# Performance work log

Hardware: AMD Instinct MI355X
Metric: run time of the kernel (lower is better)

## Reference

```python
import jax, jax.numpy as jnp
import numpy as np

ALPHA = 0.2        # LeakyReLU negative slope
MASK_VAL = -9e15   # matches torch zero_vec constant
B, N, F, H, D = 32, 1024, 64, 3, 16  # batch, nodes, in_features, heads, head_dim


def setup_inputs() -> dict:
    key = jax.random.key(0)
    k1, k2, k3 = jax.random.split(key, 3)
    h = jax.random.normal(k1, (B, N, F), dtype=jnp.float32)
    adj = jnp.ones((N, N), dtype=jnp.float32)  # fully-connected graph ('full')
    W = jax.random.normal(k2, (H, F, D), dtype=jnp.float32) * 0.15  # ~xavier gain 1.414
    a = jax.random.normal(k3, (H, 2 * D, 1), dtype=jnp.float32) * 0.25
    return {"h": h, "adj": adj, "W": W, "a": a}


def reference(h, adj, W, a):
    # Multi-head GAT, vectorized over heads (original loops over heads).
    d = W.shape[-1]
    Wh = jnp.einsum('bnf,hfd->bhnd', h, W)              # (B,H,N,D)
    a1 = a[:, :d, 0]                                    # (H,D) -> applies to source node i
    a2 = a[:, d:, 0]                                    # (H,D) -> applies to target node j
    s1 = jnp.einsum('bhnd,hd->bhn', Wh, a1)             # (B,H,N)
    s2 = jnp.einsum('bhnd,hd->bhn', Wh, a2)             # (B,H,N)
    # e[b,h,i,j] = LeakyReLU(a1.Wh_i + a2.Wh_j) -- equivalent to the repeat/concat trick
    e = jax.nn.leaky_relu(s1[..., :, None] + s2[..., None, :], ALPHA)  # (B,H,N,N)
    e = jnp.where(adj > 0, e, MASK_VAL)
    attn = jax.nn.softmax(e, axis=-1)                   # softmax over neighbors j
    out = jnp.einsum('bhij,bhjd->bhid', attn, Wh)       # (B,H,N,D)
    # concat heads along feature dim: (B,N,H*D)
    Bn, Nn = h.shape[0], h.shape[1]
    return out.transpose(0, 2, 1, 3).reshape(Bn, Nn, -1)
```

## Files before the change

kernel.cpp:

```cpp
#include <hip/hip_runtime.h>
#include <math.h>

constexpr int Bc = 32, Nn = 1024, Fc = 64, Hc = 3, Dc = 16;
constexpr float ALPHAc = 0.2f;
constexpr float L2E    = 1.44269504088896340736f;

__device__ __forceinline__ unsigned enc_f32(float x) {
    unsigned b = __builtin_bit_cast(unsigned, x);
    return (b & 0x80000000u) ? ~b : (b | 0x80000000u);
}
__device__ __forceinline__ float dec_f32(unsigned e) {
    unsigned b = (e & 0x80000000u) ? (e ^ 0x80000000u) : ~e;
    return __builtin_bit_cast(float, b);
}

template <int CTRL, int RMASK, bool BC>
__device__ __forceinline__ float dpp_acc(float x) {
    int s = __builtin_amdgcn_update_dpp(0, __builtin_bit_cast(int, x),
                                        CTRL, RMASK, 0xF, BC);
    return x + __builtin_bit_cast(float, s);
}
__device__ __forceinline__ float wave_incl_scan(float x) {
    x = dpp_acc<0x111, 0xF, true >(x);
    x = dpp_acc<0x112, 0xF, true >(x);
    x = dpp_acc<0x114, 0xF, true >(x);
    x = dpp_acc<0x118, 0xF, true >(x);
    x = dpp_acc<0x142, 0xa, false>(x);
    x = dpp_acc<0x143, 0xc, false>(x);
    return x;
}

__global__ __launch_bounds__(1024, 1) void gat_one(
    const float* __restrict__ hbuf, const float* __restrict__ W,
    const float* __restrict__ a, const float* __restrict__ adj,
    unsigned* __restrict__ rowful, float* Whf, float* __restrict__ out)
{
    __shared__ __align__(16) float    PS[1025 * 35];
    __shared__ __align__(16) unsigned skA[Nn], skB[Nn];
    __shared__ __align__(16) float    s2o[Nn];
    __shared__ float    wtot[16][34];
    __shared__ unsigned wmiss[16];

    int bh = blockIdx.x;
    int hh = bh % Hc, b = bh / Hc;
    int t  = threadIdx.x;
    int wv = t >> 6, lane = t & 63;

    int row0 = bh * 11;
    unsigned miss = 0;
#pragma unroll
    for (int rr = 0; rr < 11; ++rr) {
        int row = row0 + rr;
        if (row < Nn) {
            float av = adj[(size_t)row * Nn + t];
            miss |= (av > 0.f) ? 0u : (1u << rr);
        }
    }
#pragma unroll
    for (int off = 1; off < 64; off <<= 1)
        miss |= (unsigned)__shfl_xor((int)miss, off, 64);
    if (lane == 0) wmiss[wv] = miss;
    __syncthreads();
    if (t < 11) {
        int row = row0 + t;
        if (row < Nn) {
            unsigned m = 0;
#pragma unroll
            for (int w2 = 0; w2 < 16; ++w2) m |= wmiss[w2];
            unsigned full = ((m >> t) & 1u) ^ 1u;
            unsigned val  = 0x5AFE0000u | ((unsigned)row << 1) | full;
            __hip_atomic_store(&rowful[row], val, __ATOMIC_RELAXED,
                               __HIP_MEMORY_SCOPE_AGENT);
        }
    }

    const float4* h4 = (const float4*)(hbuf + ((size_t)b * Nn + t) * Fc);
    const float*  Wp = W + (size_t)hh * Fc * Dc;

    float acc[Dc];
#pragma unroll
    for (int d = 0; d < Dc; ++d) acc[d] = 0.f;

#pragma unroll
    for (int q = 0; q < Fc / 4; ++q) {
        float4 hv = h4[q];
#pragma unroll
        for (int c = 0; c < 4; ++c) {
            float hv1 = (c == 0) ? hv.x : (c == 1) ? hv.y : (c == 2) ? hv.z : hv.w;
            const float4* wrp = (const float4*)(Wp + (4 * q + c) * Dc);
#pragma unroll
            for (int u = 0; u < 4; ++u) {
                float4 wq = wrp[u];
                acc[4*u+0] = fmaf(hv1, wq.x, acc[4*u+0]);
                acc[4*u+1] = fmaf(hv1, wq.y, acc[4*u+1]);
                acc[4*u+2] = fmaf(hv1, wq.z, acc[4*u+2]);
                acc[4*u+3] = fmaf(hv1, wq.w, acc[4*u+3]);
            }
        }
    }

    float4* wf = (float4*)(Whf + ((size_t)bh * Nn + t) * Dc);
#pragma unroll
    for (int u = 0; u < 4; ++u)
        wf[u] = make_float4(acc[4*u+0], acc[4*u+1], acc[4*u+2], acc[4*u+3]);

    const float* ap = a + (size_t)hh * 2 * Dc;
    float s1v = 0.f, s2v = 0.f;
#pragma unroll
    for (int d = 0; d < Dc; ++d) {
        s1v = fmaf(acc[d], ap[d],      s1v);
        s2v = fmaf(acc[d], ap[Dc + d], s2v);
    }
    s2o[t] = s2v;

    unsigned key = (enc_f32(s2v) & ~1023u) | (unsigned)t;

#pragma unroll
    for (int k = 2; k <= 64; k <<= 1) {
#pragma unroll
        for (int s = k >> 1; s >= 1; s >>= 1) {
            unsigned other = (unsigned)__shfl_xor((int)key, s, 64);
            bool dirUp = ((t & k) == 0);
            bool lower = ((lane & s) == 0);
            unsigned mn = key < other ? key : other;
            unsigned mx = key < other ? other : key;
            key = (lower == dirUp) ? mn : mx;
        }
    }
    unsigned* bufs[2] = {skA, skB};
    int pb = 0;
#pragma unroll
    for (int k = 128; k <= 1024; k <<= 1) {
#pragma unroll
        for (int s = k >> 1; s >= 64; s >>= 1) {
            bufs[pb][t] = key;
            __syncthreads();
            unsigned other = bufs[pb][t ^ s];
            bool dirUp = ((t & k) == 0);
            bool lower = ((t & s) == 0);
            unsigned mn = key < other ? key : other;
            unsigned mx = key < other ? other : key;
            key = (lower == dirUp) ? mn : mx;
            pb ^= 1;
        }
#pragma unroll
        for (int s = 32; s >= 1; s >>= 1) {
            unsigned other = (unsigned)__shfl_xor((int)key, s, 64);
            bool dirUp = ((t & k) == 0);
            bool lower = ((lane & s) == 0);
            unsigned mn = key < other ? key : other;
            unsigned mx = key < other ? other : key;
            key = (lower == dirUp) ? mn : mx;
        }
    }
    unsigned* sorted = bufs[pb];
    sorted[t] = key;

    int   j  = key & 1023u;
    float sv = dec_f32((key & ~1023u) | 512u);
    float Bv = __builtin_amdgcn_exp2f(sv * L2E);
    float Dv = __builtin_amdgcn_exp2f(sv * (ALPHAc * L2E));
    const float4* wr = (const float4*)(Whf + ((size_t)bh * Nn + j) * Dc);
    float4 w0 = wr[0], w1 = wr[1], w2 = wr[2], w3 = wr[3];
    float wh[16] = {w0.x,w0.y,w0.z,w0.w, w1.x,w1.y,w1.z,w1.w,
                    w2.x,w2.y,w2.z,w2.w, w3.x,w3.y,w3.z,w3.w};

    float v[34];
#pragma unroll
    for (int d = 0; d < 16; ++d) {
        v[d]      = Bv * wh[d];
        v[16 + d] = Dv * wh[d];
    }
    v[32] = Bv; v[33] = Dv;

#pragma unroll
    for (int c = 0; c < 34; ++c) {
        float inc = wave_incl_scan(v[c]);
        if (lane == 63) wtot[wv][c] = inc;
        v[c] = inc - v[c];
    }
    __syncthreads();

    if (t < 544) {
        int c = t >> 4, w = t & 15;
        float own = wtot[w][c];
        float x = own;
#pragma unroll
        for (int off = 1; off < 16; off <<= 1) {
            float o = __shfl_up(x, off, 16);
            if ((lane & 15) >= off) x += o;
        }
        wtot[w][c] = x - own;
        if (w == 15) PS[(size_t)1024 * 35 + c] = x;
    }
    __syncthreads();

    float* myrow = PS + (size_t)t * 35;
#pragma unroll
    for (int c = 0; c < 34; ++c)
        myrow[c] = v[c] + wtot[wv][c];
    __syncthreads();

    int i = t;
    float R  = __builtin_amdgcn_exp2f(-0.8f * L2E * s1v);
    float* op = out + ((size_t)b * Nn + i) * (Hc * Dc) + hh * Dc;

    unsigned expv = 0x5AFE0000u | ((unsigned)i << 1) | 1u;
    unsigned fv;
    do {
        fv = __hip_atomic_load(&rowful[i], __ATOMIC_RELAXED,
                               __HIP_MEMORY_SCOPE_AGENT);
    } while ((fv | 1u) != expv);

    if (fv & 1u) {
        unsigned qk = (enc_f32(-s1v) & ~1023u) | 1023u;
        int p = 0;
#pragma unroll
        for (int step = 512; step >= 1; step >>= 1)
            if (sorted[p + step - 1] <= qk) p += step;

        const float* Pp = PS + (size_t)p * 35;
        const float* Tp = PS + (size_t)1024 * 35;
        float den = (Tp[32] - Pp[32]) + R * Pp[33];
        float inv = 1.0f / den;
#pragma unroll
        for (int u = 0; u < 4; ++u) {
            float o0 = ((Tp[4*u+0] - Pp[4*u+0]) + R * Pp[16 + 4*u+0]) * inv;
            float o1 = ((Tp[4*u+1] - Pp[4*u+1]) + R * Pp[16 + 4*u+1]) * inv;
            float o2 = ((Tp[4*u+2] - Pp[4*u+2]) + R * Pp[16 + 4*u+2]) * inv;
            float o3 = ((Tp[4*u+3] - Pp[4*u+3]) + R * Pp[16 + 4*u+3]) * inv;
            ((float4*)op)[u] = make_float4(o0, o1, o2, o3);
        }
    } else {
        float num[16];
#pragma unroll
        for (int d = 0; d < 16; ++d) num[d] = 0.f;
        float den = 0.f;
        for (int q = 0; q < Nn; ++q) {
            float aq = adj[(size_t)i * Nn + q];
            if (aq > 0.f) {
                float sq = s2o[q];
                float Bq = __builtin_amdgcn_exp2f(sq * L2E);
                float Dq = __builtin_amdgcn_exp2f(sq * (ALPHAc * L2E));
                float w_ = fmaxf(Bq, R * Dq);
                den += w_;
                const float* wq = Whf + ((size_t)bh * Nn + q) * Dc;
#pragma unroll
                for (int d = 0; d < 16; ++d)
                    num[d] = fmaf(w_, wq[d], num[d]);
            }
        }
        float inv = 1.0f / den;
#pragma unroll
        for (int d = 0; d < 16; ++d) op[d] = num[d] * inv;
    }
}

extern "C" void kernel_launch(void* const* d_in, const int* in_sizes, int n_in,
                              void* d_out, int out_size, void* d_ws, size_t ws_size,
                              hipStream_t stream)
{
    const float* hbuf = (const float*)d_in[0];
    const float* adj  = (const float*)d_in[1];
    const float* W    = (const float*)d_in[2];
    const float* a    = (const float*)d_in[3];
    float* out = (float*)d_out;

    float* Whf       = (float*)d_ws;
    unsigned* rowful = (unsigned*)(Whf + (size_t)Bc * Hc * Nn * Dc);

    gat_one<<<dim3(Bc * Hc), dim3(1024), 0, stream>>>(
        hbuf, W, a, adj, rowful, Whf, out);
}
```

Measured before the change: 34.85 us.

## Split each (batch,head) across four blocks by output-column quarter, keep Wh in LDS

The grid grows from B*H to 4*B*H blocks, with each block producing 4 of the 16 head-dim output columns. The sort and Wh projection are recomputed per block, but the prefix-scan width drops from 34 to 10 channels and LDS use shrinks. Wh now lives in shared memory, so the global workspace write and the gather through global memory are gone. Each block redoes the projection and bitonic sort, so that work is repeated four times. More blocks can now spread across the CUs, and the fence-free spin-wait on rowful now covers more blocks.

Result: slower. 41.40 us (+18.8%).

```diff
diff --git a/kernel.cpp b/kernel.cpp
--- a/kernel.cpp
+++ b/kernel.cpp
@@ -30,26 +30,28 @@
     return x;
 }
 
-__global__ __launch_bounds__(1024, 1) void gat_one(
+__global__ __launch_bounds__(1024, 8) void gat_one(
     const float* __restrict__ hbuf, const float* __restrict__ W,
     const float* __restrict__ a, const float* __restrict__ adj,
-    unsigned* __restrict__ rowful, float* Whf, float* __restrict__ out)
+    unsigned* __restrict__ rowful, float* __restrict__ out)
 {
-    __shared__ __align__(16) float    PS[1025 * 35];
+    __shared__ __align__(16) float    PS[1025 * 11];
     __shared__ __align__(16) unsigned skA[Nn], skB[Nn];
     __shared__ __align__(16) float    s2o[Nn];
-    __shared__ float    wtot[16][34];
+    __shared__ __align__(16) float    whs[Nn][5];
+    __shared__ float    wtot[16][10];
     __shared__ unsigned wmiss[16];
 
-    int bh = blockIdx.x;
-    int hh = bh % Hc, b = bh / Hc;
-    int t  = threadIdx.x;
-    int wv = t >> 6, lane = t & 63;
-
-    int row0 = bh * 11;
+    int gid = blockIdx.x;
+    int bh  = gid >> 2, q = gid & 3;
+    int hh  = bh % Hc,  b = bh / Hc;
+    int t   = threadIdx.x;
+    int wv  = t >> 6, lane = t & 63;
+
+    int row0 = gid * 3;
     unsigned miss = 0;
 #pragma unroll
-    for (int rr = 0; rr < 11; ++rr) {
+    for (int rr = 0; rr < 3; ++rr) {
         int row = row0 + rr;
         if (row < Nn) {
             float av = adj[(size_t)row * Nn + t];
@@ -61,7 +63,7 @@
         miss |= (unsigned)__shfl_xor((int)miss, off, 64);
     if (lane == 0) wmiss[wv] = miss;
     __syncthreads();
-    if (t < 11) {
+    if (t < 3) {
         int row = row0 + t;
         if (row < Nn) {
             unsigned m = 0;
@@ -82,12 +84,12 @@
     for (int d = 0; d < Dc; ++d) acc[d] = 0.f;
 
 #pragma unroll
-    for (int q = 0; q < Fc / 4; ++q) {
-        float4 hv = h4[q];
+    for (int qq = 0; qq < Fc / 4; ++qq) {
+        float4 hv = h4[qq];
 #pragma unroll
         for (int c = 0; c < 4; ++c) {
             float hv1 = (c == 0) ? hv.x : (c == 1) ? hv.y : (c == 2) ? hv.z : hv.w;
-            const float4* wrp = (const float4*)(Wp + (4 * q + c) * Dc);
+            const float4* wrp = (const float4*)(Wp + (4 * qq + c) * Dc);
 #pragma unroll
             for (int u = 0; u < 4; ++u) {
                 float4 wq = wrp[u];
@@ -99,10 +101,9 @@
         }
     }
 
-    float4* wf = (float4*)(Whf + ((size_t)bh * Nn + t) * Dc);
-#pragma unroll
-    for (int u = 0; u < 4; ++u)
-        wf[u] = make_float4(acc[4*u+0], acc[4*u+1], acc[4*u+2], acc[4*u+3]);
+#pragma unroll
+    for (int c = 0; c < 4; ++c)
+        whs[t][c] = acc[q * 4 + c];
 
     const float* ap = a + (size_t)hh * 2 * Dc;
     float s1v = 0.f, s2v = 0.f;
@@ -160,28 +161,20 @@
     float sv = dec_f32((key & ~1023u) | 512u);
     float Bv = __builtin_amdgcn_exp2f(sv * L2E);
     float Dv = __builtin_amdgcn_exp2f(sv * (ALPHAc * L2E));
-    const float4* wr = (const float4*)(Whf + ((size_t)bh * Nn + j) * Dc);
-    float4 w0 = wr[0], w1 = wr[1], w2 = wr[2], w3 = wr[3];
-    float wh[16] = {w0.x,w0.y,w0.z,w0.w, w1.x,w1.y,w1.z,w1.w,
-                    w2.x,w2.y,w2.z,w2.w, w3.x,w3.y,w3.z,w3.w};
-
-    float v[34];
-#pragma unroll
-    for (int d = 0; d < 16; ++d) {
-        v[d]      = Bv * wh[d];
-        v[16 + d] = Dv * wh[d];
-    }
-    v[32] = Bv; v[33] = Dv;
-
-#pragma unroll
-    for (int c = 0; c < 34; ++c) {
+    float w0 = whs[j][0], w1 = whs[j][1], w2 = whs[j][2], w3 = whs[j][3];
+
+    float v[10] = {Bv * w0, Bv * w1, Bv * w2, Bv * w3,
+                   Dv * w0, Dv * w1, Dv * w2, Dv * w3, Bv, Dv};
+
+#pragma unroll
+    for (int c = 0; c < 10; ++c) {
         float inc = wave_incl_scan(v[c]);
         if (lane == 63) wtot[wv][c] = inc;
         v[c] = inc - v[c];
     }
     __syncthreads();
 
-    if (t < 544) {
+    if (t < 160) {
         int c = t >> 4, w = t & 15;
         float own = wtot[w][c];
         float x = own;
@@ -191,19 +184,19 @@
             if ((lane & 15) >= off) x += o;
         }
         wtot[w][c] = x - own;
-        if (w == 15) PS[(size_t)1024 * 35 + c] = x;
-    }
-    __syncthreads();
-
-    float* myrow = PS + (size_t)t * 35;
-#pragma unroll
-    for (int c = 0; c < 34; ++c)
+        if (w == 15) PS[(size_t)1024 * 11 + c] = x;
+    }
+    __syncthreads();
+
+    float* myrow = PS + (size_t)t * 11;
+#pragma unroll
+    for (int c = 0; c < 10; ++c)
         myrow[c] = v[c] + wtot[wv][c];
     __syncthreads();
 
     int i = t;
     float R  = __builtin_amdgcn_exp2f(-0.8f * L2E * s1v);
-    float* op = out + ((size_t)b * Nn + i) * (Hc * Dc) + hh * Dc;
+    float* op = out + ((size_t)b * Nn + i) * (Hc * Dc) + hh * Dc + q * 4;
 
     unsigned expv = 0x5AFE0000u | ((unsigned)i << 1) | 1u;
     unsigned fv;
@@ -219,40 +212,33 @@
         for (int step = 512; step >= 1; step >>= 1)
             if (sorted[p + step - 1] <= qk) p += step;
 
-        const float* Pp = PS + (size_t)p * 35;
-        const float* Tp = PS + (size_t)1024 * 35;
-        float den = (Tp[32] - Pp[32]) + R * Pp[33];
+        const float* Pp = PS + (size_t)p * 11;
+        const float* Tp = PS + (size_t)1024 * 11;
+        float den = (Tp[8] - Pp[8]) + R * Pp[9];
         float inv = 1.0f / den;
-#pragma unroll
-        for (int u = 0; u < 4; ++u) {
-            float o0 = ((Tp[4*u+0] - Pp[4*u+0]) + R * Pp[16 + 4*u+0]) * inv;
-            float o1 = ((Tp[4*u+1] - Pp[4*u+1]) + R * Pp[16 + 4*u+1]) * inv;
-            float o2 = ((Tp[4*u+2] - Pp[4*u+2]) + R * Pp[16 + 4*u+2]) * inv;
-            float o3 = ((Tp[4*u+3] - Pp[4*u+3]) + R * Pp[16 + 4*u+3]) * inv;
-            ((float4*)op)[u] = make_float4(o0, o1, o2, o3);
-        }
+        float o0 = ((Tp[0] - Pp[0]) + R * Pp[4]) * inv;
+        float o1 = ((Tp[1] - Pp[1]) + R * Pp[5]) * inv;
+        float o2 = ((Tp[2] - Pp[2]) + R * Pp[6]) * inv;
+        float o3 = ((Tp[3] - Pp[3]) + R * Pp[7]) * inv;
+        *(float4*)op = make_float4(o0, o1, o2, o3);
     } else {
-        float num[16];
-#pragma unroll
-        for (int d = 0; d < 16; ++d) num[d] = 0.f;
+        float num[4] = {0.f, 0.f, 0.f, 0.f};
         float den = 0.f;
-        for (int q = 0; q < Nn; ++q) {
-            float aq = adj[(size_t)i * Nn + q];
+        for (int jj = 0; jj < Nn; ++jj) {
+            float aq = adj[(size_t)i * Nn + jj];
             if (aq > 0.f) {
-                float sq = s2o[q];
+                float sq = s2o[jj];
                 float Bq = __builtin_amdgcn_exp2f(sq * L2E);
                 float Dq = __builtin_amdgcn_exp2f(sq * (ALPHAc * L2E));
                 float w_ = fmaxf(Bq, R * Dq);
                 den += w_;
-                const float* wq = Whf + ((size_t)bh * Nn + q) * Dc;
-#pragma unroll
-                for (int d = 0; d < 16; ++d)
-                    num[d] = fmaf(w_, wq[d], num[d]);
+#pragma unroll
+                for (int c = 0; c < 4; ++c)
+                    num[c] = fmaf(w_, whs[jj][c], num[c]);
             }
         }
         float inv = 1.0f / den;
-#pragma unroll
-        for (int d = 0; d < 16; ++d) op[d] = num[d] * inv;
+        *(float4*)op = make_float4(num[0]*inv, num[1]*inv, num[2]*inv, num[3]*inv);
     }
 }
 
@@ -266,9 +252,8 @@
     const float* a    = (const float*)d_in[3];
     float* out = (float*)d_out;
 
-    float* Whf       = (float*)d_ws;
-    unsigned* rowful = (unsigned*)(Whf + (size_t)Bc * Hc * Nn * Dc);
-
-    gat_one<<<dim3(Bc * Hc), dim3(1024), 0, stream>>>(
-        hbuf, W, a, adj, rowful, Whf, out);
-}
+    unsigned* rowful = (unsigned*)d_ws;
+
+    gat_one<<<dim3(Bc * Hc * 4), dim3(1024), 0, stream>>>(
+        hbuf, W, a, adj, rowful, out);
+}
```
